# Kernel tuning notes

Measured on AMD Instinct MI355X. Metric: run time of the kernel, lower is better.

## Reference

```python
import jax, jax.numpy as jnp
import numpy as np

N = 8192
IN_FEATS = 256
D = IN_FEATS // 4  # 64, bottleneck dim
HID = 64           # MLP hidden_dim
K_MAX = 9
K_EC = 20
SLOPE = 0.01       # torch LeakyReLU default


def _leaky(x):
    return jnp.where(x >= 0, x, SLOPE * x)


def _knn_idx(f, k):
    # f: [N, d]; returns [N, k] indices of k nearest (incl. self, dist 0), ascending distance
    sq = jnp.sum(f * f, axis=1)
    dist = sq[:, None] + sq[None, :] - 2.0 * (f @ f.T)  # [N, N]
    _, idx = jax.lax.top_k(-dist, k)
    return idx


def _edge_conv(f, idx, Wt, bt, Wp, bp, W1, b1, W2, b2):
    # f: [N, d]; idx: [N, k] neighbor (src) indices; dst is the row node.
    x_nb = f[idx]                                   # [N, k, d] gather of src feats
    theta = (f[:, None, :] - x_nb) @ Wt.T + bt      # v_sub_u -> theta Linear
    phi = f @ Wp.T + bp                             # [N, d]
    z = phi[:, None, :] + theta                     # [N, k, d]
    # MLP(hidden=64, 2 layers, leaky_relu, activation_first=True)
    z = _leaky(z) @ W1.T + b1
    z = _leaky(z) @ W2.T + b2
    return jnp.max(z, axis=1)                       # max aggregation per dst


def _lin_init(key, out_dim, in_dim):
    k1, k2 = jax.random.split(key)
    bound = 1.0 / np.sqrt(in_dim)
    W = jax.random.uniform(k1, (out_dim, in_dim), jnp.float32, -bound, bound)
    b = jax.random.uniform(k2, (out_dim,), jnp.float32, -bound, bound)
    return W, b


def setup_inputs() -> dict:
    key = jax.random.key(0)
    keys = jax.random.split(key, 12)
    inp = {"feature": jax.random.normal(keys[0], (N, IN_FEATS), jnp.float32)}
    inp["Wb"], inp["bb"] = _lin_init(keys[1], D, IN_FEATS)
    inp["Wt1"], inp["bt1"] = _lin_init(keys[2], D, D)
    inp["Wp1"], inp["bp1"] = _lin_init(keys[3], D, D)
    inp["Wm1a"], inp["bm1a"] = _lin_init(keys[4], HID, D)
    inp["Wm1b"], inp["bm1b"] = _lin_init(keys[5], D, HID)
    inp["Wt2"], inp["bt2"] = _lin_init(keys[6], D, D)
    inp["Wp2"], inp["bp2"] = _lin_init(keys[7], D, D)
    inp["Wm2a"], inp["bm2a"] = _lin_init(keys[8], HID, D)
    inp["Wm2b"], inp["bm2b"] = _lin_init(keys[9], D, HID)
    inp["Wl"], inp["bl"] = _lin_init(keys[10], IN_FEATS, 3 * D)
    return inp


def reference(feature, Wb, bb, Wt1, bt1, Wp1, bp1, Wm1a, bm1a, Wm1b, bm1b,
              Wt2, bt2, Wp2, bp2, Wm2a, bm2a, Wm2b, bm2b, Wl, bl):
    f = feature @ Wb.T + bb                          # bottleneck [N, D]
    # KNN indices are non-differentiable (torch topk indices) -> stop_gradient
    idx40 = _knn_idx(jax.lax.stop_gradient(f), K_EC * 2)  # 40-NN, ascending distance
    idx9 = idx40[:, :K_MAX]
    idx20 = idx40[:, :K_EC]            # dilation 1
    idx20_d2 = idx40[:, ::2]           # dilation 2: every 2nd of 40-NN
    h_max = jnp.max(f[idx9], axis=1)   # copy_u + max over 9-NN
    h1 = _edge_conv(f, idx20, Wt1, bt1, Wp1, bp1, Wm1a, bm1a, Wm1b, bm1b)
    h2 = _edge_conv(f, idx20_d2, Wt2, bt2, Wp2, bp2, Wm2a, bm2a, Wm2b, bm2b)
    h = jnp.concatenate([h1, h2, h_max], axis=1) @ Wl.T + bl
    return h + feature                 # residual
```

## Files before the change

### kernel.cpp

```cpp
#include <hip/hip_runtime.h>
#include <math.h>

#define NPT   8192
#define FIN   256
#define DD    64
#define KSEL  48
#define QT    16
#define BCAP  128

#define LEAKY(x) (((x) >= 0.f) ? (x) : 0.01f*(x))

using short8v = __attribute__((ext_vector_type(8))) short;
using f32x4   = __attribute__((ext_vector_type(4))) float;

__device__ inline unsigned short f2bf(float x) {
  union { float f; unsigned u; } v; v.f = x;
  unsigned r = v.u + 0x7fff + ((v.u >> 16) & 1);
  return (unsigned short)(r >> 16);
}
__device__ inline float bf2f(unsigned short h) {
  union { unsigned u; float f; } v; v.u = ((unsigned)h) << 16; return v.f;
}
__device__ inline unsigned key_of(float f) {
  unsigned u = __float_as_uint(f);
  return (u & 0x80000000u) ? ~u : (u | 0x80000000u);
}
__device__ inline float key_inv(unsigned k) {
  unsigned u = (k >> 31) ? (k ^ 0x80000000u) : ~k;
  return __uint_as_float(u);
}

__device__ __attribute__((noinline)) void select48(
    float* __restrict__ bufd, int* __restrict__ bufi,
    int l, int n, int* bc, float* thr)
{
  float d0 = bufd[l];
  float d1 = bufd[64 + l];
  int   i0 = bufi[l];
  int   i1 = bufi[64 + l];
  unsigned k0 = (l < n)      ? key_of(d0) : 0xFFFFFFFFu;
  unsigned k1 = (64 + l < n) ? key_of(d1) : 0xFFFFFFFFu;
  unsigned prefix = 0; int need = KSEL;
  #pragma unroll
  for (int b = 31; b >= 0; --b) {
    unsigned p2 = prefix << 1;
    int c = __popcll(__ballot((k0 >> b) == p2)) +
            __popcll(__ballot((k1 >> b) == p2));
    if (c >= need) prefix = p2; else { prefix = p2 | 1u; need -= c; }
  }
  unsigned long long blt0 = __ballot(k0 < prefix), blt1 = __ballot(k1 < prefix);
  unsigned long long beq0 = __ballot(k0 == prefix), beq1 = __ballot(k1 == prefix);
  const int s = __popcll(blt0) + __popcll(blt1);
  const int tneed = KSEL - s;
  const unsigned long long below = (1ull << l) - 1ull;
  if (k0 < prefix) {
    int dst = __popcll(blt0 & below);
    bufd[dst] = d0; bufi[dst] = i0;
  } else if (k0 == prefix) {
    int r = __popcll(beq0 & below);
    if (r < tneed) { bufd[s + r] = d0; bufi[s + r] = i0; }
  }
  if (k1 < prefix) {
    int dst = __popcll(blt0) + __popcll(blt1 & below);
    bufd[dst] = d1; bufi[dst] = i1;
  } else if (k1 == prefix) {
    int r = __popcll(beq0) + __popcll(beq1 & below);
    if (r < tneed) { bufd[s + r] = d1; bufi[s + r] = i1; }
  }
  *bc = KSEL;
  *thr = key_inv(prefix);
}

__global__ void k0_prep(const float* __restrict__ Wl, const float* __restrict__ Wb,
                        const float* __restrict__ Wt1, const float* __restrict__ Wp1,
                        const float* __restrict__ Wt2, const float* __restrict__ Wp2,
                        float* __restrict__ WlT, float* __restrict__ WbT,
                        float* __restrict__ WtT1, float* __restrict__ WpT1,
                        float* __restrict__ WtT2, float* __restrict__ WpT2)
{
  const int b = blockIdx.x, t = threadIdx.x;
  if (b < 192) {
    WlT[b*256 + t] = Wl[t*192 + b];
  } else if (b < 256) {
    int j = (b - 192)*4 + (t >> 6), o = t & 63;
    WbT[j*64 + o] = Wb[o*256 + j];
  } else {
    int m = b - 256;
    const float* src = (m==0) ? Wt1 : (m==1) ? Wp1 : (m==2) ? Wt2 : Wp2;
    float*       dst = (m==0) ? WtT1: (m==1) ? WpT1: (m==2) ? WtT2: WpT2;
    #pragma unroll
    for (int i = 0; i < 16; ++i) {
      int idx = t + 256*i, r = idx >> 6, c = idx & 63;
      dst[c*64 + r] = src[r*64 + c];
    }
  }
}

__global__ __launch_bounds__(256) void k1_precompute(
    const float* __restrict__ feature, const float* __restrict__ WbT, const float* __restrict__ bb,
    const float* __restrict__ WtT1, const float* __restrict__ bt1,
    const float* __restrict__ WpT1, const float* __restrict__ bp1,
    const float* __restrict__ WtT2, const float* __restrict__ bt2,
    const float* __restrict__ WpT2, const float* __restrict__ bp2,
    double* __restrict__ f64d, double* __restrict__ sq64,
    float* __restrict__ f32v, float* __restrict__ sqf,
    float* __restrict__ u1, float* __restrict__ c1,
    float* __restrict__ u2, float* __restrict__ c2)
{
  __shared__ float f_s[4*64];
  const int w = threadIdx.x >> 6, l = threadIdx.x & 63;
  const int i = blockIdx.x*4 + w;
  const float* frow = feature + i*FIN;
  double a0 = (double)bb[l], a1 = 0.0, a2 = 0.0, a3 = 0.0;
  #pragma unroll 2
  for (int j = 0; j < FIN; j += 4) {
    float4 fv = *(const float4*)&frow[j];
    a0 += (double)fv.x * (double)WbT[(j+0)*64 + l];
    a1 += (double)fv.y * (double)WbT[(j+1)*64 + l];
    a2 += (double)fv.z * (double)WbT[(j+2)*64 + l];
    a3 += (double)fv.w * (double)WbT[(j+3)*64 + l];
  }
  double facc = (a0 + a1) + (a2 + a3);
  f64d[i*DD + l] = facc;
  float f32 = (float)facc;
  f32v[i*DD + l] = f32;
  double s = facc*facc;
  #pragma unroll
  for (int off = 32; off; off >>= 1) s += __shfl_xor(s, off);
  if (l == 0) { sq64[i] = s; sqf[i] = (float)s; }
  f_s[w*64 + l] = f32;
  float au1 = 0.f, ap1 = 0.f, au2 = 0.f, ap2 = 0.f;
  for (int e = 0; e < DD; ++e) {
    float fe = f_s[w*64 + e];
    au1 += fe * WtT1[e*64 + l];
    ap1 += fe * WpT1[e*64 + l];
    au2 += fe * WtT2[e*64 + l];
    ap2 += fe * WpT2[e*64 + l];
  }
  u1[i*DD+l] = au1;
  c1[i*DD+l] = ap1 + bp1[l] + au1 + bt1[l];
  u2[i*DD+l] = au2;
  c2[i*DD+l] = ap2 + bp2[l] + au2 + bt2[l];
}

__global__ __launch_bounds__(256) void k1b_frag(
    const float* __restrict__ f32v,
    unsigned short* __restrict__ Saf, unsigned short* __restrict__ Sbf)
{
  const int w = threadIdx.x >> 6, l = threadIdx.x & 63;
  const int task = blockIdx.x*4 + w;
  const int tile = task / 6, ks = task % 6;
  const int row  = tile*16 + (l & 15);
  const int inner = (ks & 1)*32 + ((l >> 4) << 3);
  union { unsigned short u[8]; short8v v; } pa, pb;
  #pragma unroll
  for (int j = 0; j < 8; ++j) {
    float x = f32v[row*64 + inner + j];
    unsigned short hi = f2bf(x);
    unsigned short lo = f2bf(x - bf2f(hi));
    pa.u[j] = (ks < 4) ? hi : lo;
    pb.u[j] = (ks < 2) ? hi : ((ks < 4) ? lo : hi);
  }
  size_t off = ((size_t)(tile*6 + ks)*64 + l)*8;
  *(short8v*)&Saf[off] = pa.v;
  *(short8v*)&Sbf[off] = pb.v;
}

__global__ __launch_bounds__(256) void k1c_wfrag(
    const float* __restrict__ Wm1a, const float* __restrict__ Wm1b,
    const float* __restrict__ Wm2a, const float* __restrict__ Wm2b,
    unsigned short* __restrict__ F1a, unsigned short* __restrict__ F1b,
    unsigned short* __restrict__ F2a, unsigned short* __restrict__ F2b)
{
  const int w = threadIdx.x >> 6, l = threadIdx.x & 63;
  const int task = blockIdx.x*4 + w;
  const int which = task / 24, rem = task % 24;
  const int nt = rem / 6, ks = rem % 6;
  const float* W = (which==0) ? Wm1a : (which==1) ? Wm1b : (which==2) ? Wm2a : Wm2b;
  unsigned short* F = (which==0) ? F1a : (which==1) ? F1b : (which==2) ? F2a : F2b;
  const int row = nt*16 + (l & 15);
  const int inner = (ks & 1)*32 + ((l >> 4) << 3);
  union { unsigned short u[8]; short8v v; } p;
  #pragma unroll
  for (int j = 0; j < 8; ++j) {
    float x = W[row*64 + inner + j];
    unsigned short hi = f2bf(x);
    unsigned short lo = f2bf(x - bf2f(hi));
    p.u[j] = (ks < 2) ? hi : ((ks < 4) ? lo : hi);
  }
  *(short8v*)&F[((size_t)(nt*6 + ks)*64 + l)*8] = p.v;
}

__global__ __launch_bounds__(512) void k2_knn(
    const unsigned short* __restrict__ Saf,
    const unsigned short* __restrict__ Sbf,
    const float* __restrict__ sqf,
    int* __restrict__ idx48)
{
  __shared__ float dist_s[2][QT*132];
  __shared__ float buf_d[QT*BCAP];
  __shared__ int   buf_i[QT*BCAP];

  const int t = threadIdx.x;
  const int w = t >> 6, l = t & 63;
  const int qbase = blockIdx.x * QT;

  short8v afr[4];
  {
    const size_t b = (size_t)blockIdx.x*6;
    afr[0] = *(const short8v*)&Saf[((b+0)*64 + l)*8];
    afr[1] = *(const short8v*)&Saf[((b+1)*64 + l)*8];
    afr[2] = *(const short8v*)&Saf[((b+4)*64 + l)*8];
    afr[3] = *(const short8v*)&Saf[((b+5)*64 + l)*8];
  }
  short8v bfr[4];
  {
    const size_t b = (size_t)w*6;
    #pragma unroll
    for (int s = 0; s < 4; ++s)
      bfr[s] = *(const short8v*)&Sbf[((b+s)*64 + l)*8];
  }

  float thr[2] = {__builtin_inff(), __builtin_inff()};
  int   bc[2] = {0, 0};

  for (int cb = 0; cb < NPT/128; ++cb) {
    const int jbase = cb*128;
    const float sc = sqf[jbase + w*16 + (l & 15)];
    f32x4 acc = {0.f, 0.f, 0.f, 0.f};
    acc = __builtin_amdgcn_mfma_f32_16x16x32_bf16(afr[0], bfr[0], acc, 0, 0, 0);
    acc = __builtin_amdgcn_mfma_f32_16x16x32_bf16(afr[1], bfr[1], acc, 0, 0, 0);
    acc = __builtin_amdgcn_mfma_f32_16x16x32_bf16(afr[0], bfr[2], acc, 0, 0, 0);
    acc = __builtin_amdgcn_mfma_f32_16x16x32_bf16(afr[1], bfr[3], acc, 0, 0, 0);
    acc = __builtin_amdgcn_mfma_f32_16x16x32_bf16(afr[2], bfr[0], acc, 0, 0, 0);
    acc = __builtin_amdgcn_mfma_f32_16x16x32_bf16(afr[3], bfr[1], acc, 0, 0, 0);
    if (cb < NPT/128 - 1) {
      const size_t b = (size_t)((cb+1)*8 + w)*6;
      #pragma unroll
      for (int s = 0; s < 4; ++s)
        bfr[s] = *(const short8v*)&Sbf[((b+s)*64 + l)*8];
    }
    {
      const int ncol = w*16 + (l & 15);
      #pragma unroll
      for (int r = 0; r < 4; ++r) {
        const int qrow = ((l >> 4)*4) + r;
        dist_s[cb&1][qrow*132 + ncol] = sc - 2.0f*acc[r];
      }
    }
    __syncthreads();
    #pragma unroll
    for (int qq = 0; qq < 2; ++qq) {
      const int q = 2*w + qq;
      float* bufd = &buf_d[q*BCAP];
      int*   bufi = &buf_i[q*BCAP];
      float dA = dist_s[cb&1][q*132 + l];
      float dB = dist_s[cb&1][q*132 + 64 + l];
      #pragma unroll
      for (int half = 0; half < 2; ++half) {
        float d = half ? dB : dA;
        bool pass = d < thr[qq];
        unsigned long long m = __ballot(pass);
        if (m) {
          int cnt = __popcll(m);
          if (bc[qq] + cnt > BCAP) {
            select48(bufd, bufi, l, bc[qq], &bc[qq], &thr[qq]);
            pass = d < thr[qq];
            m = __ballot(pass);
            cnt = __popcll(m);
          }
          if (pass) {
            int slot = bc[qq] + __popcll(m & ((1ull << l) - 1ull));
            bufd[slot] = d;
            bufi[slot] = jbase + 64*half + l;
          }
          bc[qq] += cnt;
        }
      }
    }
  }
  #pragma unroll
  for (int qq = 0; qq < 2; ++qq) {
    const int q = 2*w + qq;
    float* bufd = &buf_d[q*BCAP];
    int*   bufi = &buf_i[q*BCAP];
    if (bc[qq] > KSEL) select48(bufd, bufi, l, bc[qq], &bc[qq], &thr[qq]);
    if (l < KSEL) idx48[(qbase + q)*KSEL + l] = bufi[l];
  }
}

__global__ __launch_bounds__(256) void k2b_rerank(
    const double* __restrict__ f64d, const double* __restrict__ sq64,
    const int* __restrict__ idx48, int* __restrict__ idx40)
{
  __shared__ double sbd[4*KSEL];
  __shared__ int    sbi[4*KSEL];
  const int w = threadIdx.x >> 6, l = threadIdx.x & 63;
  const int node = blockIdx.x*4 + w;
  double dm = 0.0; int cand = 0;
  if (l < KSEL) {
    cand = idx48[node*KSEL + l];
    const double* fi = f64d + (size_t)node*DD;
    const double* fc = f64d + (size_t)cand*DD;
    double a0 = 0.0, a1 = 0.0;
    #pragma unroll 8
    for (int d = 0; d < DD; d += 2) { a0 += fi[d]*fc[d]; a1 += fi[d+1]*fc[d+1]; }
    dm = sq64[node] + sq64[cand] - 2.0*(a0 + a1);
    sbd[w*KSEL + l] = dm; sbi[w*KSEL + l] = cand;
  }
  __syncthreads();
  if (l < KSEL) {
    int rank = 0;
    for (int j = 0; j < KSEL; ++j) {
      double dj = sbd[w*KSEL + j];
      int    ij = sbi[w*KSEL + j];
      rank += (dj < dm) || (dj == dm && ij < cand);
    }
    if (rank < 40) idx40[node*40 + rank] = cand;
  }
}

__device__ __forceinline__ void build_frags(const float* __restrict__ zs, int mt, int l,
                                            short8v fr[4]) {
  const int row = mt*16 + (l & 15);
  const int base = row*68 + ((l >> 4) << 3);
  union { unsigned short u[8]; short8v v; } h0, h1, q0, q1;
  #pragma unroll
  for (int j = 0; j < 8; ++j) {
    float x0 = zs[base + j];
    float x1 = zs[base + 32 + j];
    unsigned short a = f2bf(x0);
    unsigned short b = f2bf(x1);
    h0.u[j] = a; q0.u[j] = f2bf(x0 - bf2f(a));
    h1.u[j] = b; q1.u[j] = f2bf(x1 - bf2f(b));
  }
  fr[0] = h0.v; fr[1] = h1.v; fr[2] = q0.v; fr[3] = q1.v;
}

#define MFMA6(ACC, AF, W0, W1, W2, W3)                                          \
  ACC = __builtin_amdgcn_mfma_f32_16x16x32_bf16(AF[0], W0, ACC, 0, 0, 0);       \
  ACC = __builtin_amdgcn_mfma_f32_16x16x32_bf16(AF[1], W1, ACC, 0, 0, 0);       \
  ACC = __builtin_amdgcn_mfma_f32_16x16x32_bf16(AF[0], W2, ACC, 0, 0, 0);       \
  ACC = __builtin_amdgcn_mfma_f32_16x16x32_bf16(AF[1], W3, ACC, 0, 0, 0);       \
  ACC = __builtin_amdgcn_mfma_f32_16x16x32_bf16(AF[2], W0, ACC, 0, 0, 0);       \
  ACC = __builtin_amdgcn_mfma_f32_16x16x32_bf16(AF[3], W1, ACC, 0, 0, 0);

__global__ __launch_bounds__(256) void k3_edgeconv(
    const float* __restrict__ f32v,
    const float* __restrict__ u1, const float* __restrict__ c1,
    const float* __restrict__ u2, const float* __restrict__ c2,
    const unsigned short* __restrict__ F1a, const unsigned short* __restrict__ F1b,
    const unsigned short* __restrict__ F2a, const unsigned short* __restrict__ F2b,
    const float* __restrict__ bm1a, const float* __restrict__ bm1b,
    const float* __restrict__ bm2a, const float* __restrict__ bm2b,
    const int* __restrict__ idx40, float* __restrict__ hout)
{
  __shared__ __align__(16) float z_s[32*68];
  __shared__ __align__(16) float a_s[32*68];
  __shared__ float red_s[2*64];
  __shared__ int idx_sh[40];
  const int t = threadIdx.x, i = blockIdx.x;
  const int w = t >> 6, l = t & 63;
  const int mt = w >> 1;
  const int nb0 = (w & 1)*2;
  if (t < 40) idx_sh[t] = idx40[i*40 + t];
  __syncthreads();

  for (int conv = 0; conv < 2; ++conv) {
    const float* u_g = conv ? u2 : u1;
    const float* c_g = conv ? c2 : c1;
    const unsigned short* WfA = conv ? F2a : F1a;
    const unsigned short* WfB = conv ? F2b : F1b;
    const float* bav = conv ? bm2a : bm1a;
    const float* bbv = conv ? bm2b : bm1b;
    #pragma unroll
    for (int r = 0; r < 8; ++r) {
      int flat = t + 256*r, row = flat >> 6, d = flat & 63;
      float z = 0.f;
      if (row < 20) {
        int nb = idx_sh[conv ? 2*row : row];
        float zv = c_g[i*DD + d] - u_g[nb*DD + d];
        z = LEAKY(zv);
      }
      z_s[row*68 + d] = z;
    }
    __syncthreads();
    short8v afr[4];
    build_frags(z_s, mt, l, afr);
    f32x4 acc0 = {0.f,0.f,0.f,0.f}, acc1 = {0.f,0.f,0.f,0.f};
    {
      const unsigned short* p0 = WfA + ((size_t)(nb0+0)*6*64)*8;
      const unsigned short* p1 = WfA + ((size_t)(nb0+1)*6*64)*8;
      short8v w00 = *(const short8v*)&p0[(0*64+l)*8];
      short8v w01 = *(const short8v*)&p0[(1*64+l)*8];
      short8v w02 = *(const short8v*)&p0[(2*64+l)*8];
      short8v w03 = *(const short8v*)&p0[(3*64+l)*8];
      short8v w10 = *(const short8v*)&p1[(0*64+l)*8];
      short8v w11 = *(const short8v*)&p1[(1*64+l)*8];
      short8v w12 = *(const short8v*)&p1[(2*64+l)*8];
      short8v w13 = *(const short8v*)&p1[(3*64+l)*8];
      MFMA6(acc0, afr, w00, w01, w02, w03);
      MFMA6(acc1, afr, w10, w11, w12, w13);
    }
    {
      const int c0 = (nb0+0)*16 + (l & 15), c1i = (nb0+1)*16 + (l & 15);
      const float ba0 = bav[c0], ba1 = bav[c1i];
      #pragma unroll
      for (int r = 0; r < 4; ++r) {
        const int row = mt*16 + (l >> 4)*4 + r;
        float v0 = acc0[r] + ba0;
        float v1 = acc1[r] + ba1;
        a_s[row*68 + c0]  = LEAKY(v0);
        a_s[row*68 + c1i] = LEAKY(v1);
      }
    }
    __syncthreads();
    short8v bfr[4];
    build_frags(a_s, mt, l, bfr);
    f32x4 bacc0 = {0.f,0.f,0.f,0.f}, bacc1 = {0.f,0.f,0.f,0.f};
    {
      const unsigned short* p0 = WfB + ((size_t)(nb0+0)*6*64)*8;
      const unsigned short* p1 = WfB + ((size_t)(nb0+1)*6*64)*8;
      short8v w00 = *(const short8v*)&p0[(0*64+l)*8];
      short8v w01 = *(const short8v*)&p0[(1*64+l)*8];
      short8v w02 = *(const short8v*)&p0[(2*64+l)*8];
      short8v w03 = *(const short8v*)&p0[(3*64+l)*8];
      short8v w10 = *(const short8v*)&p1[(0*64+l)*8];
      short8v w11 = *(const short8v*)&p1[(1*64+l)*8];
      short8v w12 = *(const short8v*)&p1[(2*64+l)*8];
      short8v w13 = *(const short8v*)&p1[(3*64+l)*8];
      MFMA6(bacc0, bfr, w00, w01, w02, w03);
      MFMA6(bacc1, bfr, w10, w11, w12, w13);
    }
    {
      const int c0 = (nb0+0)*16 + (l & 15), c1i = (nb0+1)*16 + (l & 15);
      const float bb0 = bbv[c0], bb1 = bbv[c1i];
      float m0 = -__builtin_inff(), m1 = -__builtin_inff();
      #pragma unroll
      for (int r = 0; r < 4; ++r) {
        const int row = mt*16 + (l >> 4)*4 + r;
        if (row < 20) {
          m0 = fmaxf(m0, bacc0[r] + bb0);
          m1 = fmaxf(m1, bacc1[r] + bb1);
        }
      }
      m0 = fmaxf(m0, __shfl_xor(m0, 16)); m0 = fmaxf(m0, __shfl_xor(m0, 32));
      m1 = fmaxf(m1, __shfl_xor(m1, 16)); m1 = fmaxf(m1, __shfl_xor(m1, 32));
      if ((l >> 4) == 0) {
        red_s[mt*64 + c0]  = m0;
        red_s[mt*64 + c1i] = m1;
      }
    }
    __syncthreads();
    if (t < 64) hout[i*192 + conv*64 + t] = fmaxf(red_s[t], red_s[64 + t]);
    __syncthreads();
  }
  if (t < 64) {
    float m = -__builtin_inff();
    #pragma unroll
    for (int k = 0; k < 9; ++k) m = fmaxf(m, f32v[idx_sh[k]*DD + t]);
    hout[i*192 + 128 + t] = m;
  }
}

__global__ __launch_bounds__(256) void k4_final(
    const float* __restrict__ hbuf, const float* __restrict__ WlT,
    const float* __restrict__ bl, const float* __restrict__ feature,
    float* __restrict__ out)
{
  __shared__ __align__(16) float h_sh[16*192];
  const int t = threadIdx.x;
  const int nbase = blockIdx.x * 16;
  #pragma unroll
  for (int r = 0; r < 3; ++r) {
    int flat = t + 256*r;
    int n = flat / 48, j4 = flat % 48;
    *(float4*)&h_sh[n*192 + 4*j4] = *(const float4*)&hbuf[(nbase+n)*192 + 4*j4];
  }
  __syncthreads();
  float acc[16];
  #pragma unroll
  for (int n = 0; n < 16; ++n) acc[n] = 0.f;
  for (int j4 = 0; j4 < 48; ++j4) {
    float w0 = WlT[(4*j4+0)*256 + t];
    float w1 = WlT[(4*j4+1)*256 + t];
    float w2 = WlT[(4*j4+2)*256 + t];
    float w3 = WlT[(4*j4+3)*256 + t];
    #pragma unroll
    for (int n = 0; n < 16; ++n) {
      float4 hv = *(const float4*)&h_sh[n*192 + 4*j4];
      acc[n] += hv.x*w0 + hv.y*w1 + hv.z*w2 + hv.w*w3;
    }
  }
  float blv = bl[t];
  #pragma unroll
  for (int n = 0; n < 16; ++n)
    out[(nbase+n)*256 + t] = acc[n] + blv + feature[(nbase+n)*256 + t];
}

extern "C" void kernel_launch(void* const* d_in, const int* in_sizes, int n_in,
                              void* d_out, int out_size, void* d_ws, size_t ws_size,
                              hipStream_t stream) {
  const float* feature = (const float*)d_in[0];
  const float* Wb   = (const float*)d_in[1];
  const float* bb   = (const float*)d_in[2];
  const float* Wt1  = (const float*)d_in[3];
  const float* bt1  = (const float*)d_in[4];
  const float* Wp1  = (const float*)d_in[5];
  const float* bp1  = (const float*)d_in[6];
  const float* Wm1a = (const float*)d_in[7];
  const float* bm1a = (const float*)d_in[8];
  const float* Wm1b = (const float*)d_in[9];
  const float* bm1b = (const float*)d_in[10];
  const float* Wt2  = (const float*)d_in[11];
  const float* bt2  = (const float*)d_in[12];
  const float* Wp2  = (const float*)d_in[13];
  const float* bp2  = (const float*)d_in[14];
  const float* Wm2a = (const float*)d_in[15];
  const float* bm2a = (const float*)d_in[16];
  const float* Wm2b = (const float*)d_in[17];
  const float* bm2b = (const float*)d_in[18];
  const float* Wl   = (const float*)d_in[19];
  const float* bl   = (const float*)d_in[20];
  float* out = (float*)d_out;

  char* ws = (char*)d_ws;
  double* f64d = (double*)(ws + 0);
  double* sq64 = (double*)(ws + 4194304);
  float*  f32v = (float*)(ws + 4259840);
  float*  sqf  = (float*)(ws + 6356992);
  float*  u1   = (float*)(ws + 6389760);
  float*  c1   = (float*)(ws + 8486912);
  float*  u2   = (float*)(ws + 10584064);
  float*  c2   = (float*)(ws + 12681216);
  int*    idx48= (int*)(ws + 14778368);
  int*    idx40= (int*)(ws + 16351232);
  float*  hbuf = (float*)(ws + 17661952);
  float*  WlT  = (float*)(ws + 23953408);
  unsigned short* Saf = (unsigned short*)(ws + 24150016);
  unsigned short* Sbf = (unsigned short*)(ws + 27295744);
  float*  WbT  = (float*)(ws + 30441472);
  float*  WtT1 = (float*)(ws + 30507008);
  float*  WpT1 = (float*)(ws + 30523392);
  float*  WtT2 = (float*)(ws + 30539776);
  float*  WpT2 = (float*)(ws + 30556160);
  unsigned short* F1a = (unsigned short*)(ws + 30572544);
  unsigned short* F1b = (unsigned short*)(ws + 30597120);
  unsigned short* F2a = (unsigned short*)(ws + 30621696);
  unsigned short* F2b = (unsigned short*)(ws + 30646272);

  hipLaunchKernelGGL(k0_prep, dim3(260), dim3(256), 0, stream,
                     Wl, Wb, Wt1, Wp1, Wt2, Wp2, WlT, WbT, WtT1, WpT1, WtT2, WpT2);
  hipLaunchKernelGGL(k1c_wfrag, dim3(24), dim3(256), 0, stream,
                     Wm1a, Wm1b, Wm2a, Wm2b, F1a, F1b, F2a, F2b);
  hipLaunchKernelGGL(k1_precompute, dim3(2048), dim3(256), 0, stream,
                     feature, WbT, bb, WtT1, bt1, WpT1, bp1, WtT2, bt2, WpT2, bp2,
                     f64d, sq64, f32v, sqf, u1, c1, u2, c2);
  hipLaunchKernelGGL(k1b_frag, dim3(768), dim3(256), 0, stream, f32v, Saf, Sbf);
  hipLaunchKernelGGL(k2_knn, dim3(NPT/QT), dim3(512), 0, stream, Saf, Sbf, sqf, idx48);
  hipLaunchKernelGGL(k2b_rerank, dim3(2048), dim3(256), 0, stream, f64d, sq64, idx48, idx40);
  hipLaunchKernelGGL(k3_edgeconv, dim3(8192), dim3(256), 0, stream,
                     f32v, u1, c1, u2, c2, F1a, F1b, F2a, F2b,
                     bm1a, bm1b, bm2a, bm2b, idx40, hbuf);
  hipLaunchKernelGGL(k4_final, dim3(512), dim3(256), 0, stream, hbuf, WlT, bl, feature, out);
}
```

Before: 451.2 us.

## Replace streaming kNN buffer selection with sample-threshold filter and global select

The single kNN kernel, which kept a per-query shared buffer and repeatedly ran radix selection, is replaced by four stages. A sampled 1/8 of the columns sets a per-query threshold at the 41st smallest sampled distance. A filter pass then computes all distances with MFMA and appends survivors to per-query global lists through atomics, and a final radix select picks 48 candidates. The rerank kernel is also changed to one block per node with the dot products split across four threads. This trades the serialized select48 calls for extra kernel launches, a second distance GEMM over the sampled columns, global atomics and larger scratch traffic. Survivor lists are capped at 640 entries, so an unlucky threshold could drop true neighbours.

```diff
diff --git a/kernel.cpp b/kernel.cpp
--- a/kernel.cpp
+++ b/kernel.cpp
@@ -5,8 +5,7 @@
 #define FIN   256
 #define DD    64
 #define KSEL  48
-#define QT    16
-#define BCAP  128
+#define SCAP  640
 
 #define LEAKY(x) (((x) >= 0.f) ? (x) : 0.01f*(x))
 
@@ -28,47 +27,6 @@
 __device__ inline float key_inv(unsigned k) {
   unsigned u = (k >> 31) ? (k ^ 0x80000000u) : ~k;
   return __uint_as_float(u);
-}
-
-__device__ __attribute__((noinline)) void select48(
-    float* __restrict__ bufd, int* __restrict__ bufi,
-    int l, int n, int* bc, float* thr)
-{
-  float d0 = bufd[l];
-  float d1 = bufd[64 + l];
-  int   i0 = bufi[l];
-  int   i1 = bufi[64 + l];
-  unsigned k0 = (l < n)      ? key_of(d0) : 0xFFFFFFFFu;
-  unsigned k1 = (64 + l < n) ? key_of(d1) : 0xFFFFFFFFu;
-  unsigned prefix = 0; int need = KSEL;
-  #pragma unroll
-  for (int b = 31; b >= 0; --b) {
-    unsigned p2 = prefix << 1;
-    int c = __popcll(__ballot((k0 >> b) == p2)) +
-            __popcll(__ballot((k1 >> b) == p2));
-    if (c >= need) prefix = p2; else { prefix = p2 | 1u; need -= c; }
-  }
-  unsigned long long blt0 = __ballot(k0 < prefix), blt1 = __ballot(k1 < prefix);
-  unsigned long long beq0 = __ballot(k0 == prefix), beq1 = __ballot(k1 == prefix);
-  const int s = __popcll(blt0) + __popcll(blt1);
-  const int tneed = KSEL - s;
-  const unsigned long long below = (1ull << l) - 1ull;
-  if (k0 < prefix) {
-    int dst = __popcll(blt0 & below);
-    bufd[dst] = d0; bufi[dst] = i0;
-  } else if (k0 == prefix) {
-    int r = __popcll(beq0 & below);
-    if (r < tneed) { bufd[s + r] = d0; bufi[s + r] = i0; }
-  }
-  if (k1 < prefix) {
-    int dst = __popcll(blt0) + __popcll(blt1 & below);
-    bufd[dst] = d1; bufi[dst] = i1;
-  } else if (k1 == prefix) {
-    int r = __popcll(beq0) + __popcll(beq1 & below);
-    if (r < tneed) { bufd[s + r] = d1; bufi[s + r] = i1; }
-  }
-  *bc = KSEL;
-  *thr = key_inv(prefix);
 }
 
 __global__ void k0_prep(const float* __restrict__ Wl, const float* __restrict__ Wb,
@@ -191,132 +149,232 @@
   *(short8v*)&F[((size_t)(nt*6 + ks)*64 + l)*8] = p.v;
 }
 
-__global__ __launch_bounds__(512) void k2_knn(
+#define MFMA_PAIR6(ACC, AF, BF)                                                  \
+  ACC = __builtin_amdgcn_mfma_f32_16x16x32_bf16(AF[0], BF[0], ACC, 0, 0, 0);     \
+  ACC = __builtin_amdgcn_mfma_f32_16x16x32_bf16(AF[1], BF[1], ACC, 0, 0, 0);     \
+  ACC = __builtin_amdgcn_mfma_f32_16x16x32_bf16(AF[0], BF[2], ACC, 0, 0, 0);     \
+  ACC = __builtin_amdgcn_mfma_f32_16x16x32_bf16(AF[1], BF[3], ACC, 0, 0, 0);     \
+  ACC = __builtin_amdgcn_mfma_f32_16x16x32_bf16(AF[2], BF[0], ACC, 0, 0, 0);     \
+  ACC = __builtin_amdgcn_mfma_f32_16x16x32_bf16(AF[3], BF[1], ACC, 0, 0, 0);
+
+__global__ __launch_bounds__(512) void k2a_sample(
     const unsigned short* __restrict__ Saf,
     const unsigned short* __restrict__ Sbf,
     const float* __restrict__ sqf,
-    int* __restrict__ idx48)
-{
-  __shared__ float dist_s[2][QT*132];
-  __shared__ float buf_d[QT*BCAP];
-  __shared__ int   buf_i[QT*BCAP];
-
-  const int t = threadIdx.x;
-  const int w = t >> 6, l = t & 63;
-  const int qbase = blockIdx.x * QT;
-
-  short8v afr[4];
-  {
-    const size_t b = (size_t)blockIdx.x*6;
-    afr[0] = *(const short8v*)&Saf[((b+0)*64 + l)*8];
-    afr[1] = *(const short8v*)&Saf[((b+1)*64 + l)*8];
-    afr[2] = *(const short8v*)&Saf[((b+4)*64 + l)*8];
-    afr[3] = *(const short8v*)&Saf[((b+5)*64 + l)*8];
+    float* __restrict__ sampD)
+{
+  const int t = threadIdx.x, w = t >> 6, l = t & 63;
+  const int qbase = blockIdx.x * 32;
+  short8v afr[2][4];
+  #pragma unroll
+  for (int mt = 0; mt < 2; ++mt) {
+    const size_t b = (size_t)(blockIdx.x*2 + mt)*6;
+    afr[mt][0] = *(const short8v*)&Saf[((b+0)*64 + l)*8];
+    afr[mt][1] = *(const short8v*)&Saf[((b+1)*64 + l)*8];
+    afr[mt][2] = *(const short8v*)&Saf[((b+4)*64 + l)*8];
+    afr[mt][3] = *(const short8v*)&Saf[((b+5)*64 + l)*8];
+  }
+  const int ncol = w*16 + (l & 15);
+  for (int s = 0; s < 8; ++s) {
+    const int cb = s*8;
+    const int jbase = cb*128;
+    short8v bfr[4];
+    {
+      const size_t b = (size_t)(cb*8 + w)*6;
+      #pragma unroll
+      for (int k = 0; k < 4; ++k)
+        bfr[k] = *(const short8v*)&Sbf[((b+k)*64 + l)*8];
+    }
+    const float sc = sqf[jbase + ncol];
+    f32x4 acc0 = {0.f,0.f,0.f,0.f}, acc1 = {0.f,0.f,0.f,0.f};
+    MFMA_PAIR6(acc0, afr[0], bfr);
+    MFMA_PAIR6(acc1, afr[1], bfr);
+    #pragma unroll
+    for (int r = 0; r < 4; ++r) {
+      const int q0 = qbase + 0*16 + (l >> 4)*4 + r;
+      const int q1 = qbase + 1*16 + (l >> 4)*4 + r;
+      sampD[(size_t)q0*1024 + s*128 + ncol] = sc - 2.0f*acc0[r];
+      sampD[(size_t)q1*1024 + s*128 + ncol] = sc - 2.0f*acc1[r];
+    }
+  }
+}
+
+__global__ __launch_bounds__(256) void k2t_threshold(
+    const float* __restrict__ sampD, float* __restrict__ Tq, int* __restrict__ cnt_g)
+{
+  const int w = threadIdx.x >> 6, l = threadIdx.x & 63;
+  const int q = blockIdx.x*4 + w;
+  unsigned ku[16];
+  #pragma unroll
+  for (int k = 0; k < 16; ++k)
+    ku[k] = key_of(sampD[(size_t)q*1024 + k*64 + l]);
+  unsigned prefix = 0; int need = 41;
+  for (int b = 31; b >= 0; --b) {
+    unsigned p2 = prefix << 1;
+    int c = 0;
+    #pragma unroll
+    for (int k = 0; k < 16; ++k) c += ((ku[k] >> b) == p2);
+    #pragma unroll
+    for (int off = 32; off; off >>= 1) c += __shfl_xor(c, off);
+    if (c >= need) prefix = p2; else { prefix = p2 | 1u; need -= c; }
+  }
+  if (l == 0) { Tq[q] = key_inv(prefix); cnt_g[q] = 0; }
+}
+
+__global__ __launch_bounds__(512) void k2f_filter(
+    const unsigned short* __restrict__ Saf,
+    const unsigned short* __restrict__ Sbf,
+    const float* __restrict__ sqf,
+    const float* __restrict__ Tq,
+    int* __restrict__ cnt_g,
+    float* __restrict__ survD, int* __restrict__ survI)
+{
+  const int t = threadIdx.x, w = t >> 6, l = t & 63;
+  const int qbase = blockIdx.x * 32;
+  short8v afr[2][4];
+  float Tr[2][4]; int qg[2][4];
+  #pragma unroll
+  for (int mt = 0; mt < 2; ++mt) {
+    const size_t b = (size_t)(blockIdx.x*2 + mt)*6;
+    afr[mt][0] = *(const short8v*)&Saf[((b+0)*64 + l)*8];
+    afr[mt][1] = *(const short8v*)&Saf[((b+1)*64 + l)*8];
+    afr[mt][2] = *(const short8v*)&Saf[((b+4)*64 + l)*8];
+    afr[mt][3] = *(const short8v*)&Saf[((b+5)*64 + l)*8];
+    #pragma unroll
+    for (int r = 0; r < 4; ++r) {
+      int q = qbase + mt*16 + (l >> 4)*4 + r;
+      qg[mt][r] = q;
+      Tr[mt][r] = Tq[q];
+    }
   }
   short8v bfr[4];
   {
     const size_t b = (size_t)w*6;
     #pragma unroll
-    for (int s = 0; s < 4; ++s)
-      bfr[s] = *(const short8v*)&Sbf[((b+s)*64 + l)*8];
-  }
-
-  float thr[2] = {__builtin_inff(), __builtin_inff()};
-  int   bc[2] = {0, 0};
-
+    for (int k = 0; k < 4; ++k)
+      bfr[k] = *(const short8v*)&Sbf[((b+k)*64 + l)*8];
+  }
+  const int ncol = w*16 + (l & 15);
   for (int cb = 0; cb < NPT/128; ++cb) {
     const int jbase = cb*128;
-    const float sc = sqf[jbase + w*16 + (l & 15)];
-    f32x4 acc = {0.f, 0.f, 0.f, 0.f};
-    acc = __builtin_amdgcn_mfma_f32_16x16x32_bf16(afr[0], bfr[0], acc, 0, 0, 0);
-    acc = __builtin_amdgcn_mfma_f32_16x16x32_bf16(afr[1], bfr[1], acc, 0, 0, 0);
-    acc = __builtin_amdgcn_mfma_f32_16x16x32_bf16(afr[0], bfr[2], acc, 0, 0, 0);
-    acc = __builtin_amdgcn_mfma_f32_16x16x32_bf16(afr[1], bfr[3], acc, 0, 0, 0);
-    acc = __builtin_amdgcn_mfma_f32_16x16x32_bf16(afr[2], bfr[0], acc, 0, 0, 0);
-    acc = __builtin_amdgcn_mfma_f32_16x16x32_bf16(afr[3], bfr[1], acc, 0, 0, 0);
+    const float sc = sqf[jbase + ncol];
+    f32x4 acc0 = {0.f,0.f,0.f,0.f}, acc1 = {0.f,0.f,0.f,0.f};
+    MFMA_PAIR6(acc0, afr[0], bfr);
+    MFMA_PAIR6(acc1, afr[1], bfr);
     if (cb < NPT/128 - 1) {
       const size_t b = (size_t)((cb+1)*8 + w)*6;
       #pragma unroll
-      for (int s = 0; s < 4; ++s)
-        bfr[s] = *(const short8v*)&Sbf[((b+s)*64 + l)*8];
-    }
-    {
-      const int ncol = w*16 + (l & 15);
-      #pragma unroll
-      for (int r = 0; r < 4; ++r) {
-        const int qrow = ((l >> 4)*4) + r;
-        dist_s[cb&1][qrow*132 + ncol] = sc - 2.0f*acc[r];
-      }
-    }
-    __syncthreads();
-    #pragma unroll
-    for (int qq = 0; qq < 2; ++qq) {
-      const int q = 2*w + qq;
-      float* bufd = &buf_d[q*BCAP];
-      int*   bufi = &buf_i[q*BCAP];
-      float dA = dist_s[cb&1][q*132 + l];
-      float dB = dist_s[cb&1][q*132 + 64 + l];
-      #pragma unroll
-      for (int half = 0; half < 2; ++half) {
-        float d = half ? dB : dA;
-        bool pass = d < thr[qq];
-        unsigned long long m = __ballot(pass);
-        if (m) {
-          int cnt = __popcll(m);
-          if (bc[qq] + cnt > BCAP) {
-            select48(bufd, bufi, l, bc[qq], &bc[qq], &thr[qq]);
-            pass = d < thr[qq];
-            m = __ballot(pass);
-            cnt = __popcll(m);
-          }
-          if (pass) {
-            int slot = bc[qq] + __popcll(m & ((1ull << l) - 1ull));
-            bufd[slot] = d;
-            bufi[slot] = jbase + 64*half + l;
-          }
-          bc[qq] += cnt;
+      for (int k = 0; k < 4; ++k)
+        bfr[k] = *(const short8v*)&Sbf[((b+k)*64 + l)*8];
+    }
+    const int j = jbase + ncol;
+    #pragma unroll
+    for (int r = 0; r < 4; ++r) {
+      float d0 = sc - 2.0f*acc0[r];
+      if (d0 < Tr[0][r]) {
+        int slot = atomicAdd(&cnt_g[qg[0][r]], 1);
+        if (slot < SCAP) {
+          survD[(size_t)qg[0][r]*SCAP + slot] = d0;
+          survI[(size_t)qg[0][r]*SCAP + slot] = j;
         }
       }
-    }
-  }
-  #pragma unroll
-  for (int qq = 0; qq < 2; ++qq) {
-    const int q = 2*w + qq;
-    float* bufd = &buf_d[q*BCAP];
-    int*   bufi = &buf_i[q*BCAP];
-    if (bc[qq] > KSEL) select48(bufd, bufi, l, bc[qq], &bc[qq], &thr[qq]);
-    if (l < KSEL) idx48[(qbase + q)*KSEL + l] = bufi[l];
-  }
-}
-
-__global__ __launch_bounds__(256) void k2b_rerank(
+      float d1 = sc - 2.0f*acc1[r];
+      if (d1 < Tr[1][r]) {
+        int slot = atomicAdd(&cnt_g[qg[1][r]], 1);
+        if (slot < SCAP) {
+          survD[(size_t)qg[1][r]*SCAP + slot] = d1;
+          survI[(size_t)qg[1][r]*SCAP + slot] = j;
+        }
+      }
+    }
+  }
+}
+
+__global__ __launch_bounds__(256) void k2s_select(
+    const float* __restrict__ survD, const int* __restrict__ survI,
+    const int* __restrict__ cnt_g, int* __restrict__ idx48)
+{
+  const int w = threadIdx.x >> 6, l = threadIdx.x & 63;
+  const int node = blockIdx.x*4 + w;
+  const int n = min(cnt_g[node], SCAP);
+  unsigned ku[10]; int iv[10];
+  #pragma unroll
+  for (int k = 0; k < 10; ++k) {
+    int e = k*64 + l;
+    bool v = e < n;
+    float d = v ? survD[(size_t)node*SCAP + e] : 0.f;
+    iv[k] = v ? survI[(size_t)node*SCAP + e] : 0;
+    ku[k] = v ? key_of(d) : 0xFFFFFFFFu;
+  }
+  unsigned prefix = 0; int need = KSEL;
+  for (int b = 31; b >= 0; --b) {
+    unsigned p2 = prefix << 1;
+    int c = 0;
+    #pragma unroll
+    for (int k = 0; k < 10; ++k) c += ((ku[k] >> b) == p2);
+    #pragma unroll
+    for (int off = 32; off; off >>= 1) c += __shfl_xor(c, off);
+    if (c >= need) prefix = p2; else { prefix = p2 | 1u; need -= c; }
+  }
+  const unsigned long long below = (1ull << l) - 1ull;
+  int base = 0;
+  #pragma unroll
+  for (int k = 0; k < 10; ++k) {
+    unsigned long long blt = __ballot(ku[k] < prefix);
+    if (ku[k] < prefix) {
+      int pos = base + __popcll(blt & below);
+      idx48[(size_t)node*KSEL + pos] = iv[k];
+    }
+    base += __popcll(blt);
+  }
+  #pragma unroll
+  for (int k = 0; k < 10; ++k) {
+    unsigned long long beq = __ballot(ku[k] == prefix);
+    if (ku[k] == prefix) {
+      int pos = base + __popcll(beq & below);
+      if (pos < KSEL) idx48[(size_t)node*KSEL + pos] = iv[k];
+    }
+    base += __popcll(beq);
+  }
+}
+
+__global__ __launch_bounds__(256) void k2r_rerank(
     const double* __restrict__ f64d, const double* __restrict__ sq64,
     const int* __restrict__ idx48, int* __restrict__ idx40)
 {
-  __shared__ double sbd[4*KSEL];
-  __shared__ int    sbi[4*KSEL];
-  const int w = threadIdx.x >> 6, l = threadIdx.x & 63;
-  const int node = blockIdx.x*4 + w;
-  double dm = 0.0; int cand = 0;
-  if (l < KSEL) {
-    cand = idx48[node*KSEL + l];
-    const double* fi = f64d + (size_t)node*DD;
-    const double* fc = f64d + (size_t)cand*DD;
+  __shared__ double part[KSEL][4];
+  __shared__ double dist_sh[KSEL];
+  __shared__ int    cand_sh[KSEL];
+  const int t = threadIdx.x;
+  const int node = blockIdx.x;
+  if (t < KSEL) cand_sh[t] = idx48[(size_t)node*KSEL + t];
+  __syncthreads();
+  if (t < 192) {
+    int c = t >> 2, qt = t & 3;
+    int cand = cand_sh[c];
+    const double* fi = f64d + (size_t)node*DD + qt*16;
+    const double* fc = f64d + (size_t)cand*DD + qt*16;
     double a0 = 0.0, a1 = 0.0;
-    #pragma unroll 8
-    for (int d = 0; d < DD; d += 2) { a0 += fi[d]*fc[d]; a1 += fi[d+1]*fc[d+1]; }
-    dm = sq64[node] + sq64[cand] - 2.0*(a0 + a1);
-    sbd[w*KSEL + l] = dm; sbi[w*KSEL + l] = cand;
+    #pragma unroll
+    for (int d = 0; d < 16; d += 2) { a0 += fi[d]*fc[d]; a1 += fi[d+1]*fc[d+1]; }
+    part[c][qt] = a0 + a1;
   }
   __syncthreads();
-  if (l < KSEL) {
+  if (t < KSEL) {
+    int cand = cand_sh[t];
+    dist_sh[t] = sq64[node] + sq64[cand]
+               - 2.0*(part[t][0] + part[t][1] + part[t][2] + part[t][3]);
+  }
+  __syncthreads();
+  if (t < KSEL) {
+    double dm = dist_sh[t]; int cand = cand_sh[t];
     int rank = 0;
     for (int j = 0; j < KSEL; ++j) {
-      double dj = sbd[w*KSEL + j];
-      int    ij = sbi[w*KSEL + j];
+      double dj = dist_sh[j];
+      int    ij = cand_sh[j];
       rank += (dj < dm) || (dj == dm && ij < cand);
     }
-    if (rank < 40) idx40[node*40 + rank] = cand;
+    if (rank < 40) idx40[(size_t)node*40 + rank] = cand;
   }
 }
 
@@ -548,6 +606,11 @@
   unsigned short* F1b = (unsigned short*)(ws + 30597120);
   unsigned short* F2a = (unsigned short*)(ws + 30621696);
   unsigned short* F2b = (unsigned short*)(ws + 30646272);
+  float*  Tq   = (float*)(ws + 30670848);
+  int*    cnt_g= (int*)(ws + 30703616);
+  float*  survD= (float*)(ws + 30736384);
+  int*    survI= (int*)(ws + 51707904);
+  float*  sampD= (float*)(ws + 30736384);
 
   hipLaunchKernelGGL(k0_prep, dim3(260), dim3(256), 0, stream,
                      Wl, Wb, Wt1, Wp1, Wt2, Wp2, WlT, WbT, WtT1, WpT1, WtT2, WpT2);
@@ -557,8 +620,12 @@
                      feature, WbT, bb, WtT1, bt1, WpT1, bp1, WtT2, bt2, WpT2, bp2,
                      f64d, sq64, f32v, sqf, u1, c1, u2, c2);
   hipLaunchKernelGGL(k1b_frag, dim3(768), dim3(256), 0, stream, f32v, Saf, Sbf);
-  hipLaunchKernelGGL(k2_knn, dim3(NPT/QT), dim3(512), 0, stream, Saf, Sbf, sqf, idx48);
-  hipLaunchKernelGGL(k2b_rerank, dim3(2048), dim3(256), 0, stream, f64d, sq64, idx48, idx40);
+  hipLaunchKernelGGL(k2a_sample, dim3(256), dim3(512), 0, stream, Saf, Sbf, sqf, sampD);
+  hipLaunchKernelGGL(k2t_threshold, dim3(2048), dim3(256), 0, stream, sampD, Tq, cnt_g);
+  hipLaunchKernelGGL(k2f_filter, dim3(256), dim3(512), 0, stream,
+                     Saf, Sbf, sqf, Tq, cnt_g, survD, survI);
+  hipLaunchKernelGGL(k2s_select, dim3(2048), dim3(256), 0, stream, survD, survI, cnt_g, idx48);
+  hipLaunchKernelGGL(k2r_rerank, dim3(8192), dim3(256), 0, stream, f64d, sq64, idx48, idx40);
   hipLaunchKernelGGL(k3_edgeconv, dim3(8192), dim3(256), 0, stream,
                      f32v, u1, c1, u2, c2, F1a, F1b, F2a, F2b,
                      bm1a, bm1b, bm2a, bm2b, idx40, hbuf);
```

Measured after the change: 608.1 us. 1.35x slower.
